# Optimization experiments

Hardware: AMD Instinct MI355X
Metric: run time of the kernel (lower is better)

Reference implementation:

```python
import jax, jax.numpy as jnp
import numpy as np

N_NODES = 50000
NEG_SLOPE = 0.2


def gat_conv(x, src, dst, W, a_src, a_dst, bias, heads):
    # x: [N, Fin]; W: [Fin, heads*C]; a_src/a_dst: [heads, C]; bias: [heads*C]
    n = x.shape[0]
    h = (x @ W).reshape(n, heads, -1)              # [N, H, C]
    alpha_src = jnp.einsum('nhc,hc->nh', h, a_src)  # [N, H]
    alpha_dst = jnp.einsum('nhc,hc->nh', h, a_dst)  # [N, H]
    e = alpha_src[src] + alpha_dst[dst]             # [E, H]
    e = jax.nn.leaky_relu(e, NEG_SLOPE)
    # segment softmax over edges grouped by destination node
    m = jax.ops.segment_max(e, dst, num_segments=n)          # [N, H]
    e = jnp.exp(e - jax.lax.stop_gradient(m)[dst])
    s = jax.ops.segment_sum(e, dst, num_segments=n)          # [N, H]
    alpha = e / (s[dst] + 1e-16)                              # [E, H]
    msg = h[src] * alpha[:, :, None]                          # [E, H, C]
    out = jax.ops.segment_sum(msg, dst, num_segments=n)      # [N, H, C]
    return out.reshape(n, -1) + bias


def add_self_loops(edge_index, n):
    loops = jnp.arange(n, dtype=edge_index.dtype)
    src = jnp.concatenate([edge_index[0], loops])
    dst = jnp.concatenate([edge_index[1], loops])
    return src, dst


def setup_inputs() -> dict:
    key = jax.random.key(0)
    ks = jax.random.split(key, 10)
    num_features, num_classes, heads1, c1 = 128, 40, 8, 32
    n_edges = 800000
    x = jax.random.normal(ks[0], (N_NODES, num_features), dtype=jnp.float32)
    edge_index = jax.random.randint(ks[1], (2, n_edges), 0, N_NODES, dtype=jnp.int64)
    sc = 0.1
    W1 = jax.random.normal(ks[2], (num_features, heads1 * c1), dtype=jnp.float32) * sc
    a_src1 = jax.random.normal(ks[3], (heads1, c1), dtype=jnp.float32) * sc
    a_dst1 = jax.random.normal(ks[4], (heads1, c1), dtype=jnp.float32) * sc
    b1 = jnp.zeros((heads1 * c1,), dtype=jnp.float32)
    W2 = jax.random.normal(ks[5], (heads1 * c1, num_classes), dtype=jnp.float32) * sc
    a_src2 = jax.random.normal(ks[6], (1, num_classes), dtype=jnp.float32) * sc
    a_dst2 = jax.random.normal(ks[7], (1, num_classes), dtype=jnp.float32) * sc
    b2 = jnp.zeros((num_classes,), dtype=jnp.float32)
    return {"x": x, "edge_index": edge_index, "W1": W1, "a_src1": a_src1,
            "a_dst1": a_dst1, "b1": b1, "W2": W2, "a_src2": a_src2,
            "a_dst2": a_dst2, "b2": b2}


def reference(x, edge_index, W1, a_src1, a_dst1, b1, W2, a_src2, a_dst2, b2):
    src, dst = add_self_loops(edge_index, x.shape[0])
    h = gat_conv(x, src, dst, W1, a_src1, a_dst1, b1, heads=8)
    h = jax.nn.elu(h)
    h = gat_conv(h, src, dst, W2, a_src2, a_dst2, b2, heads=1)
    return jax.nn.log_softmax(h, axis=1)
```

## Files before the change

kernel.cpp:

```cpp
#include <hip/hip_runtime.h>
#include <math.h>

#define NNODES 50000
#define F_IN   128
#define F1     256
#define H1N    8
#define NCLS   40
#define NEG    0.2f
#define MNEG  -3.0e38f
#define SCAN_BLOCKS 196

typedef unsigned int uint32;
typedef __attribute__((ext_vector_type(8))) short short8v;
typedef __attribute__((ext_vector_type(4))) float f32x4;

__device__ __forceinline__ float leaky(float x) { return x > 0.f ? x : NEG * x; }

__device__ __forceinline__ unsigned short f2bf(float f) {
  uint32 u = __float_as_uint(f);
  u = (u + 0x7FFFu + ((u >> 16) & 1u)) >> 16;
  return (unsigned short)u;
}
__device__ __forceinline__ float bf_lo(uint32 u) { return __uint_as_float(u << 16); }
__device__ __forceinline__ float bf_hi(uint32 u) { return __uint_as_float(u & 0xFFFF0000u); }

__global__ __launch_bounds__(256) void convx_k(const float* __restrict__ x,
                                               unsigned short* __restrict__ xb) {
  int i = blockIdx.x * 256 + threadIdx.x;
  float4 v = ((const float4*)x)[i];
  uint2 o;
  o.x = (uint32)f2bf(v.x) | ((uint32)f2bf(v.y) << 16);
  o.y = (uint32)f2bf(v.z) | ((uint32)f2bf(v.w) << 16);
  ((uint2*)xb)[i] = o;
}

__global__ __launch_bounds__(256) void convw_k(const float* __restrict__ W,
                                               unsigned short* __restrict__ Wt) {
  int id = blockIdx.x * 256 + threadIdx.x;
  int k = id >> 8, c = id & 255;
  Wt[c * 128 + k] = f2bf(W[id]);
}

__global__ __launch_bounds__(256) void convw2_k(const float* __restrict__ W2,
                                                unsigned short* __restrict__ Wt2) {
  int id = blockIdx.x * 256 + threadIdx.x;
  int c = id >> 8, k = id & 255;
  Wt2[c * 256 + k] = (c < NCLS) ? f2bf(W2[k * NCLS + c]) : (unsigned short)0;
}

__global__ __launch_bounds__(256) void gemm1_mfma_k(
    const unsigned short* __restrict__ xb, const unsigned short* __restrict__ Wt,
    const float* __restrict__ asrc, const float* __restrict__ adst,
    unsigned short* __restrict__ h1b, float* __restrict__ as1,
    float* __restrict__ ad1) {
  const int lane = threadIdx.x & 63;
  const int wv   = threadIdx.x >> 6;
  const int row0 = blockIdx.x * 64 + wv * 16;
  if (row0 >= NNODES) return;
  const int lrow = lane & 15;
  const int kgrp = lane >> 4;

  const short8v* xp = (const short8v*)xb;
  short8v a[4];
  #pragma unroll
  for (int ks = 0; ks < 4; ++ks)
    a[ks] = xp[(row0 + lrow) * 16 + ks * 4 + kgrp];

  const short8v* wp = (const short8v*)Wt;
  float ps[4] = {0.f, 0.f, 0.f, 0.f};
  float pd[4] = {0.f, 0.f, 0.f, 0.f};

  for (int n = 0; n < 16; ++n) {
    f32x4 acc = {0.f, 0.f, 0.f, 0.f};
    #pragma unroll
    for (int ks = 0; ks < 4; ++ks) {
      short8v b = wp[(n * 16 + lrow) * 16 + ks * 4 + kgrp];
      acc = __builtin_amdgcn_mfma_f32_16x16x32_bf16(a[ks], b, acc, 0, 0, 0);
    }
    const int col = n * 16 + lrow;
    const float ascv = asrc[col];
    const float advv = adst[col];
    #pragma unroll
    for (int r = 0; r < 4; ++r) {
      int row = row0 + kgrp * 4 + r;
      h1b[(long)row * F1 + col] = f2bf(acc[r]);
      ps[r] = fmaf(acc[r], ascv, ps[r]);
      pd[r] = fmaf(acc[r], advv, pd[r]);
    }
    if (n & 1) {
      const int head = n >> 1;
      #pragma unroll
      for (int r = 0; r < 4; ++r) {
        #pragma unroll
        for (int mask = 1; mask <= 8; mask <<= 1) {
          ps[r] += __shfl_xor(ps[r], mask, 64);
          pd[r] += __shfl_xor(pd[r], mask, 64);
        }
      }
      if (lrow == 0) {
        #pragma unroll
        for (int r = 0; r < 4; ++r) {
          int row = row0 + kgrp * 4 + r;
          as1[row * H1N + head] = ps[r];
          ad1[row * H1N + head] = pd[r];
        }
      }
      #pragma unroll
      for (int r = 0; r < 4; ++r) { ps[r] = 0.f; pd[r] = 0.f; }
    }
  }
}

__global__ __launch_bounds__(256) void hist_k(const int* __restrict__ ei,
                                              int* __restrict__ deg, int E, int ET) {
  int e = blockIdx.x * 256 + threadIdx.x;
  if (e >= ET) return;
  int d = (e < E) ? ei[E + e] : e - E;
  atomicAdd(&deg[d], 1);
}

__global__ __launch_bounds__(256) void partsum_k(const int* __restrict__ deg,
                                                 int* __restrict__ blocksum) {
  int idx = blockIdx.x * 256 + threadIdx.x;
  int v = (idx < NNODES) ? deg[idx] : 0;
  #pragma unroll
  for (int m = 32; m >= 1; m >>= 1) v += __shfl_xor(v, m, 64);
  __shared__ int sh[4];
  if ((threadIdx.x & 63) == 0) sh[threadIdx.x >> 6] = v;
  __syncthreads();
  if (threadIdx.x == 0) blocksum[blockIdx.x] = sh[0] + sh[1] + sh[2] + sh[3];
}

__global__ __launch_bounds__(256) void scanblocks_k(const int* __restrict__ blocksum,
                                                    int* __restrict__ blockoff) {
  __shared__ int sh[256];
  int t = threadIdx.x;
  int v = (t < SCAN_BLOCKS) ? blocksum[t] : 0;
  sh[t] = v;
  __syncthreads();
  for (int off = 1; off < 256; off <<= 1) {
    int u = (t >= off) ? sh[t - off] : 0;
    __syncthreads();
    sh[t] += u;
    __syncthreads();
  }
  if (t < SCAN_BLOCKS) blockoff[t] = (t == 0) ? 0 : sh[t - 1];
}

__global__ __launch_bounds__(256) void rowstart_k(const int* __restrict__ deg,
                                                  const int* __restrict__ blockoff,
                                                  int* __restrict__ row_start,
                                                  int* __restrict__ cursor, int ET) {
  __shared__ int sh[256];
  int t = threadIdx.x;
  int idx = blockIdx.x * 256 + t;
  int v = (idx < NNODES) ? deg[idx] : 0;
  sh[t] = v;
  __syncthreads();
  for (int off = 1; off < 256; off <<= 1) {
    int u = (t >= off) ? sh[t - off] : 0;
    __syncthreads();
    sh[t] += u;
    __syncthreads();
  }
  int incl = sh[t];
  int base = blockoff[blockIdx.x];
  if (idx < NNODES) {
    int rs = base + incl - v;
    row_start[idx] = rs;
    cursor[idx] = rs;
    if (idx == NNODES - 1) row_start[NNODES] = base + incl;
  }
}

__global__ __launch_bounds__(256) void scatter_k(const int* __restrict__ ei,
                                                 int* __restrict__ cursor,
                                                 int* __restrict__ csr_src, int E, int ET) {
  int e = blockIdx.x * 256 + threadIdx.x;
  if (e >= ET) return;
  int s, d;
  if (e < E) { s = ei[e]; d = ei[E + e]; } else { s = d = e - E; }
  int pos = atomicAdd(&cursor[d], 1);
  csr_src[pos] = s;
}

__global__ __launch_bounds__(256) void att1_k(
    const int* __restrict__ row_start, const int* __restrict__ csr_src,
    const float* __restrict__ as1, const float* __restrict__ ad1,
    float* __restrict__ alpha1, float* __restrict__ r1) {
  int wave = threadIdx.x >> 6, lane = threadIdx.x & 63;
  int d = blockIdx.x * 4 + wave;
  if (d >= NNODES) return;
  int r0 = row_start[d], r1e = row_start[d + 1];
  float adv[8];
  #pragma unroll
  for (int h = 0; h < 8; ++h) adv[h] = ad1[d * 8 + h];
  float sum[8];
  #pragma unroll
  for (int h = 0; h < 8; ++h) sum[h] = 0.f;
  for (int i = r0 + lane; i < r1e; i += 64) {
    int s = csr_src[i];
    const float4* ap = (const float4*)(as1 + (long)s * 8);
    float4 a0 = ap[0], a1 = ap[1];
    float av[8] = {a0.x, a0.y, a0.z, a0.w, a1.x, a1.y, a1.z, a1.w};
    float ex[8];
    #pragma unroll
    for (int h = 0; h < 8; ++h) {
      ex[h] = __expf(leaky(av[h] + adv[h]));
      sum[h] += ex[h];
    }
    float4* op = (float4*)(alpha1 + (long)i * 8);
    op[0] = make_float4(ex[0], ex[1], ex[2], ex[3]);
    op[1] = make_float4(ex[4], ex[5], ex[6], ex[7]);
  }
  #pragma unroll
  for (int mask = 1; mask <= 32; mask <<= 1) {
    #pragma unroll
    for (int h = 0; h < 8; ++h) sum[h] += __shfl_xor(sum[h], mask, 64);
  }
  if (lane == 0) {
    #pragma unroll
    for (int h = 0; h < 8; ++h) r1[d * 8 + h] = 1.f / (sum[h] + 1e-16f);
  }
}

__global__ __launch_bounds__(128) void agg1_k(
    const int* __restrict__ row_start, const int* __restrict__ csr_src,
    const float* __restrict__ alpha1, const float* __restrict__ r1,
    const uint32* __restrict__ h1b, const float* __restrict__ b1,
    uint32* __restrict__ x2b) {
  int d = blockIdx.x;
  int t = threadIdx.x;
  int h = t >> 4;
  int r0 = row_start[d], r1e = row_start[d + 1];
  float acc0 = 0.f, acc1 = 0.f;
  int i = r0;
  for (; i + 2 <= r1e; i += 2) {
    int s0 = csr_src[i], s1 = csr_src[i + 1];
    float a0 = alpha1[(long)i * 8 + h];
    float a1 = alpha1[(long)(i + 1) * 8 + h];
    uint32 v0 = h1b[s0 * 128 + t];
    uint32 v1 = h1b[s1 * 128 + t];
    acc0 = fmaf(bf_lo(v0), a0, acc0);
    acc1 = fmaf(bf_hi(v0), a0, acc1);
    acc0 = fmaf(bf_lo(v1), a1, acc0);
    acc1 = fmaf(bf_hi(v1), a1, acc1);
  }
  if (i < r1e) {
    int s0 = csr_src[i];
    float a0 = alpha1[(long)i * 8 + h];
    uint32 v0 = h1b[s0 * 128 + t];
    acc0 = fmaf(bf_lo(v0), a0, acc0);
    acc1 = fmaf(bf_hi(v0), a0, acc1);
  }
  float rch = r1[d * 8 + h];
  acc0 *= rch;
  acc1 *= rch;
  float2 b = ((const float2*)b1)[t];
  float o0 = acc0 + b.x, o1 = acc1 + b.y;
  o0 = o0 > 0.f ? o0 : expm1f(o0);
  o1 = o1 > 0.f ? o1 : expm1f(o1);
  x2b[(long)d * 128 + t] = (uint32)f2bf(o0) | ((uint32)f2bf(o1) << 16);
}

__global__ __launch_bounds__(256) void gemm2_mfma_k(
    const unsigned short* __restrict__ x2b, const unsigned short* __restrict__ Wt2,
    const float* __restrict__ a_src2, const float* __restrict__ a_dst2,
    float* __restrict__ h2, float* __restrict__ as2, float* __restrict__ ad2) {
  const int lane = threadIdx.x & 63;
  const int wv   = threadIdx.x >> 6;
  const int row0 = blockIdx.x * 64 + wv * 16;
  if (row0 >= NNODES) return;
  const int lrow = lane & 15;
  const int kgrp = lane >> 4;

  const short8v* xp = (const short8v*)x2b;
  short8v a[8];
  #pragma unroll
  for (int ks = 0; ks < 8; ++ks)
    a[ks] = xp[(row0 + lrow) * 32 + ks * 4 + kgrp];

  const short8v* wp = (const short8v*)Wt2;
  float ps[4] = {0.f, 0.f, 0.f, 0.f};
  float pd[4] = {0.f, 0.f, 0.f, 0.f};

  #pragma unroll
  for (int n = 0; n < 3; ++n) {
    f32x4 acc = {0.f, 0.f, 0.f, 0.f};
    #pragma unroll
    for (int ks = 0; ks < 8; ++ks) {
      short8v b = wp[(n * 16 + lrow) * 32 + ks * 4 + kgrp];
      acc = __builtin_amdgcn_mfma_f32_16x16x32_bf16(a[ks], b, acc, 0, 0, 0);
    }
    const int col = n * 16 + lrow;
    const bool valid = col < NCLS;
    const float asv = valid ? a_src2[col] : 0.f;
    const float adv = valid ? a_dst2[col] : 0.f;
    #pragma unroll
    for (int r = 0; r < 4; ++r) {
      int row = row0 + kgrp * 4 + r;
      if (valid) h2[(long)row * NCLS + col] = acc[r];
      ps[r] = fmaf(acc[r], asv, ps[r]);
      pd[r] = fmaf(acc[r], adv, pd[r]);
    }
  }
  #pragma unroll
  for (int r = 0; r < 4; ++r) {
    #pragma unroll
    for (int mask = 1; mask <= 8; mask <<= 1) {
      ps[r] += __shfl_xor(ps[r], mask, 64);
      pd[r] += __shfl_xor(pd[r], mask, 64);
    }
  }
  if (lrow == 0) {
    #pragma unroll
    for (int r = 0; r < 4; ++r) {
      int row = row0 + kgrp * 4 + r;
      as2[row] = ps[r];
      ad2[row] = pd[r];
    }
  }
}

__global__ __launch_bounds__(256) void att2e_k(
    const int* __restrict__ row_start, const int* __restrict__ csr_src,
    const float* __restrict__ as2, const float* __restrict__ ad2,
    float* __restrict__ alpha2, float* __restrict__ r2) {
  int wave = threadIdx.x >> 6, lane = threadIdx.x & 63;
  int d = blockIdx.x * 4 + wave;
  if (d >= NNODES) return;
  int r0 = row_start[d], r1e = row_start[d + 1];
  float add = ad2[d];
  float sum = 0.f;
  for (int i = r0 + lane; i < r1e; i += 64) {
    float ex = __expf(leaky(as2[csr_src[i]] + add));
    alpha2[i] = ex;
    sum += ex;
  }
  #pragma unroll
  for (int mask = 1; mask <= 32; mask <<= 1) sum += __shfl_xor(sum, mask, 64);
  if (lane == 0) r2[d] = 1.f / (sum + 1e-16f);
}

__global__ __launch_bounds__(256) void agg2_k(
    const int* __restrict__ row_start, const int* __restrict__ csr_src,
    const float* __restrict__ alpha2, const float* __restrict__ r2,
    const float* __restrict__ h2, const float* __restrict__ b2,
    float* __restrict__ out) {
  int wave = threadIdx.x >> 6, lane = threadIdx.x & 63;
  int d = blockIdx.x * 4 + wave;
  if (d >= NNODES) return;
  int r0 = row_start[d], r1e = row_start[d + 1];

  float acc = 0.f;
  int i = r0;
  for (; i + 2 <= r1e; i += 2) {
    int s0 = csr_src[i], s1 = csr_src[i + 1];
    float a0 = alpha2[i], a1 = alpha2[i + 1];
    float v0 = (lane < NCLS) ? h2[(long)s0 * NCLS + lane] : 0.f;
    float v1 = (lane < NCLS) ? h2[(long)s1 * NCLS + lane] : 0.f;
    acc = fmaf(v0, a0, acc);
    acc = fmaf(v1, a1, acc);
  }
  if (i < r1e) {
    int s0 = csr_src[i];
    float a0 = alpha2[i];
    float v0 = (lane < NCLS) ? h2[(long)s0 * NCLS + lane] : 0.f;
    acc = fmaf(v0, a0, acc);
  }
  acc *= r2[d];

  float v = (lane < NCLS) ? acc + b2[lane] : MNEG;
  float mm = v;
  #pragma unroll
  for (int mask = 1; mask <= 32; mask <<= 1) mm = fmaxf(mm, __shfl_xor(mm, mask, 64));
  float ex = (lane < NCLS) ? __expf(v - mm) : 0.f;
  float se = ex;
  #pragma unroll
  for (int mask = 1; mask <= 32; mask <<= 1) se += __shfl_xor(se, mask, 64);
  if (lane < NCLS) out[(long)d * NCLS + lane] = v - mm - __logf(se);
}

extern "C" void kernel_launch(void* const* d_in, const int* in_sizes, int n_in,
                              void* d_out, int out_size, void* d_ws, size_t ws_size,
                              hipStream_t stream) {
  const float* x      = (const float*)d_in[0];
  const int*   ei     = (const int*)d_in[1];
  const float* W1     = (const float*)d_in[2];
  const float* a_src1 = (const float*)d_in[3];
  const float* a_dst1 = (const float*)d_in[4];
  const float* b1     = (const float*)d_in[5];
  const float* W2     = (const float*)d_in[6];
  const float* a_src2 = (const float*)d_in[7];
  const float* a_dst2 = (const float*)d_in[8];
  const float* b2     = (const float*)d_in[9];
  float* out = (float*)d_out;

  const int E  = in_sizes[1] / 2;
  const int ET = E + NNODES;

  float* ws = (float*)d_ws;
  unsigned short* h1b = (unsigned short*)ws;
  float* h2     = ws;
  float* as2    = ws + 2000000;
  float* ad2    = ws + 2050000;
  uint32* x2b   = (uint32*)(ws + 6400000);
  unsigned short* xb = (unsigned short*)(ws + 9700000);
  unsigned short* Wt = (unsigned short*)(ws + 13000000);
  unsigned short* Wt2 = (unsigned short*)(ws + 13100000);
  float* alpha2 = ws + 13200000;
  float* r1     = ws + 15000000;
  float* r2     = ws + 15400000;
  float* as1    = ws + 19200000;
  float* ad1    = ws + 19600000;
  float* alpha1 = ws + 20000000;
  int* row_start = (int*)(ws + 26800000);
  int* cursor    = row_start + 50001;
  int* deg       = cursor + 50000;
  int* csr_src   = deg + 50000;
  int* blocksum  = csr_src + 850000;
  int* blockoff  = blocksum + 256;

  hipMemsetAsync(deg, 0, NNODES * sizeof(int), stream);

  hist_k<<<(ET + 255) / 256, 256, 0, stream>>>(ei, deg, E, ET);
  partsum_k<<<SCAN_BLOCKS, 256, 0, stream>>>(deg, blocksum);
  scanblocks_k<<<1, 256, 0, stream>>>(blocksum, blockoff);
  rowstart_k<<<SCAN_BLOCKS, 256, 0, stream>>>(deg, blockoff, row_start, cursor, ET);
  scatter_k<<<(ET + 255) / 256, 256, 0, stream>>>(ei, cursor, csr_src, E, ET);

  convx_k<<<6250, 256, 0, stream>>>(x, xb);
  convw_k<<<128, 256, 0, stream>>>(W1, Wt);
  convw2_k<<<48, 256, 0, stream>>>(W2, Wt2);
  gemm1_mfma_k<<<(NNODES + 63) / 64, 256, 0, stream>>>(xb, Wt, a_src1, a_dst1,
                                                       h1b, as1, ad1);
  att1_k<<<NNODES / 4, 256, 0, stream>>>(row_start, csr_src, as1, ad1, alpha1, r1);
  agg1_k<<<NNODES, 128, 0, stream>>>(row_start, csr_src, alpha1, r1,
                                     (const uint32*)h1b, b1, x2b);

  gemm2_mfma_k<<<(NNODES + 63) / 64, 256, 0, stream>>>(
      (const unsigned short*)x2b, Wt2, a_src2, a_dst2, h2, as2, ad2);
  att2e_k<<<NNODES / 4, 256, 0, stream>>>(row_start, csr_src, as2, ad2, alpha2, r2);
  agg2_k<<<NNODES / 4, 256, 0, stream>>>(row_start, csr_src, alpha2, r2, h2, b2, out);
}
```

Measured before the change: 424.7 us.

## Fuse attention softmax into aggregation kernels, recomputing edge weights on the fly

The separate attention kernels for both GAT layers are removed. Each aggregation kernel now computes the per-destination softmax denominator itself, using a block reduction through LDS for layer 1 and a wave shuffle for layer 2. It then recomputes exp(leaky(as[s]+ad[d])) per edge during accumulation instead of reading stored alpha arrays. This drops the alpha1/alpha2 writes and reads (about 850K×8 floats for layer 1) and two kernel launches. In exchange it adds redundant exp computation, an extra pass over edges with gathers of as1/as2, and two __syncthreads per node in agg1.

```diff
diff --git a/kernel.cpp b/kernel.cpp
--- a/kernel.cpp
+++ b/kernel.cpp
@@ -184,61 +184,42 @@
   csr_src[pos] = s;
 }
 
-__global__ __launch_bounds__(256) void att1_k(
+__global__ __launch_bounds__(128) void agg1_k(
     const int* __restrict__ row_start, const int* __restrict__ csr_src,
     const float* __restrict__ as1, const float* __restrict__ ad1,
-    float* __restrict__ alpha1, float* __restrict__ r1) {
-  int wave = threadIdx.x >> 6, lane = threadIdx.x & 63;
-  int d = blockIdx.x * 4 + wave;
-  if (d >= NNODES) return;
-  int r0 = row_start[d], r1e = row_start[d + 1];
-  float adv[8];
-  #pragma unroll
-  for (int h = 0; h < 8; ++h) adv[h] = ad1[d * 8 + h];
-  float sum[8];
-  #pragma unroll
-  for (int h = 0; h < 8; ++h) sum[h] = 0.f;
-  for (int i = r0 + lane; i < r1e; i += 64) {
-    int s = csr_src[i];
-    const float4* ap = (const float4*)(as1 + (long)s * 8);
-    float4 a0 = ap[0], a1 = ap[1];
-    float av[8] = {a0.x, a0.y, a0.z, a0.w, a1.x, a1.y, a1.z, a1.w};
-    float ex[8];
-    #pragma unroll
-    for (int h = 0; h < 8; ++h) {
-      ex[h] = __expf(leaky(av[h] + adv[h]));
-      sum[h] += ex[h];
-    }
-    float4* op = (float4*)(alpha1 + (long)i * 8);
-    op[0] = make_float4(ex[0], ex[1], ex[2], ex[3]);
-    op[1] = make_float4(ex[4], ex[5], ex[6], ex[7]);
-  }
-  #pragma unroll
-  for (int mask = 1; mask <= 32; mask <<= 1) {
-    #pragma unroll
-    for (int h = 0; h < 8; ++h) sum[h] += __shfl_xor(sum[h], mask, 64);
-  }
-  if (lane == 0) {
-    #pragma unroll
-    for (int h = 0; h < 8; ++h) r1[d * 8 + h] = 1.f / (sum[h] + 1e-16f);
-  }
-}
-
-__global__ __launch_bounds__(128) void agg1_k(
-    const int* __restrict__ row_start, const int* __restrict__ csr_src,
-    const float* __restrict__ alpha1, const float* __restrict__ r1,
     const uint32* __restrict__ h1b, const float* __restrict__ b1,
     uint32* __restrict__ x2b) {
-  int d = blockIdx.x;
-  int t = threadIdx.x;
-  int h = t >> 4;
-  int r0 = row_start[d], r1e = row_start[d + 1];
+  __shared__ float partial[128];
+  __shared__ float rs_lds[8];
+  const int d = blockIdx.x;
+  const int t = threadIdx.x;
+  const int r0 = row_start[d], r1e = row_start[d + 1];
+
+  {
+    const int hh = t & 7, slot = t >> 3;
+    const float adv = ad1[d * 8 + hh];
+    float sum = 0.f;
+    for (int i = r0 + slot; i < r1e; i += 16)
+      sum += __expf(leaky(as1[csr_src[i] * 8 + hh] + adv));
+    partial[t] = sum;
+  }
+  __syncthreads();
+  if (t < 8) {
+    float s = 0.f;
+    #pragma unroll
+    for (int j = 0; j < 16; ++j) s += partial[t + 8 * j];
+    rs_lds[t] = 1.f / (s + 1e-16f);
+  }
+  __syncthreads();
+
+  const int h = t >> 4;
+  const float adh = ad1[d * 8 + h];
   float acc0 = 0.f, acc1 = 0.f;
   int i = r0;
   for (; i + 2 <= r1e; i += 2) {
     int s0 = csr_src[i], s1 = csr_src[i + 1];
-    float a0 = alpha1[(long)i * 8 + h];
-    float a1 = alpha1[(long)(i + 1) * 8 + h];
+    float a0 = __expf(leaky(as1[s0 * 8 + h] + adh));
+    float a1 = __expf(leaky(as1[s1 * 8 + h] + adh));
     uint32 v0 = h1b[s0 * 128 + t];
     uint32 v1 = h1b[s1 * 128 + t];
     acc0 = fmaf(bf_lo(v0), a0, acc0);
@@ -248,12 +229,12 @@
   }
   if (i < r1e) {
     int s0 = csr_src[i];
-    float a0 = alpha1[(long)i * 8 + h];
+    float a0 = __expf(leaky(as1[s0 * 8 + h] + adh));
     uint32 v0 = h1b[s0 * 128 + t];
     acc0 = fmaf(bf_lo(v0), a0, acc0);
     acc1 = fmaf(bf_hi(v0), a0, acc1);
   }
-  float rch = r1[d * 8 + h];
+  float rch = rs_lds[h];
   acc0 *= rch;
   acc1 *= rch;
   float2 b = ((const float2*)b1)[t];
@@ -322,41 +303,30 @@
   }
 }
 
-__global__ __launch_bounds__(256) void att2e_k(
+__global__ __launch_bounds__(256) void agg2_k(
     const int* __restrict__ row_start, const int* __restrict__ csr_src,
     const float* __restrict__ as2, const float* __restrict__ ad2,
-    float* __restrict__ alpha2, float* __restrict__ r2) {
-  int wave = threadIdx.x >> 6, lane = threadIdx.x & 63;
-  int d = blockIdx.x * 4 + wave;
-  if (d >= NNODES) return;
-  int r0 = row_start[d], r1e = row_start[d + 1];
-  float add = ad2[d];
-  float sum = 0.f;
-  for (int i = r0 + lane; i < r1e; i += 64) {
-    float ex = __expf(leaky(as2[csr_src[i]] + add));
-    alpha2[i] = ex;
-    sum += ex;
-  }
-  #pragma unroll
-  for (int mask = 1; mask <= 32; mask <<= 1) sum += __shfl_xor(sum, mask, 64);
-  if (lane == 0) r2[d] = 1.f / (sum + 1e-16f);
-}
-
-__global__ __launch_bounds__(256) void agg2_k(
-    const int* __restrict__ row_start, const int* __restrict__ csr_src,
-    const float* __restrict__ alpha2, const float* __restrict__ r2,
     const float* __restrict__ h2, const float* __restrict__ b2,
     float* __restrict__ out) {
   int wave = threadIdx.x >> 6, lane = threadIdx.x & 63;
   int d = blockIdx.x * 4 + wave;
   if (d >= NNODES) return;
   int r0 = row_start[d], r1e = row_start[d + 1];
+  const float add = ad2[d];
+
+  float sum = 0.f;
+  for (int i = r0 + lane; i < r1e; i += 64)
+    sum += __expf(leaky(as2[csr_src[i]] + add));
+  #pragma unroll
+  for (int mask = 1; mask <= 32; mask <<= 1) sum += __shfl_xor(sum, mask, 64);
+  float rcp = 1.f / (sum + 1e-16f);
 
   float acc = 0.f;
   int i = r0;
   for (; i + 2 <= r1e; i += 2) {
     int s0 = csr_src[i], s1 = csr_src[i + 1];
-    float a0 = alpha2[i], a1 = alpha2[i + 1];
+    float a0 = __expf(leaky(as2[s0] + add));
+    float a1 = __expf(leaky(as2[s1] + add));
     float v0 = (lane < NCLS) ? h2[(long)s0 * NCLS + lane] : 0.f;
     float v1 = (lane < NCLS) ? h2[(long)s1 * NCLS + lane] : 0.f;
     acc = fmaf(v0, a0, acc);
@@ -364,11 +334,11 @@
   }
   if (i < r1e) {
     int s0 = csr_src[i];
-    float a0 = alpha2[i];
+    float a0 = __expf(leaky(as2[s0] + add));
     float v0 = (lane < NCLS) ? h2[(long)s0 * NCLS + lane] : 0.f;
     acc = fmaf(v0, a0, acc);
   }
-  acc *= r2[d];
+  acc *= rcp;
 
   float v = (lane < NCLS) ? acc + b2[lane] : MNEG;
   float mm = v;
@@ -408,12 +378,8 @@
   unsigned short* xb = (unsigned short*)(ws + 9700000);
   unsigned short* Wt = (unsigned short*)(ws + 13000000);
   unsigned short* Wt2 = (unsigned short*)(ws + 13100000);
-  float* alpha2 = ws + 13200000;
-  float* r1     = ws + 15000000;
-  float* r2     = ws + 15400000;
   float* as1    = ws + 19200000;
   float* ad1    = ws + 19600000;
-  float* alpha1 = ws + 20000000;
   int* row_start = (int*)(ws + 26800000);
   int* cursor    = row_start + 50001;
   int* deg       = cursor + 50000;
@@ -434,12 +400,10 @@
   convw2_k<<<48, 256, 0, stream>>>(W2, Wt2);
   gemm1_mfma_k<<<(NNODES + 63) / 64, 256, 0, stream>>>(xb, Wt, a_src1, a_dst1,
                                                        h1b, as1, ad1);
-  att1_k<<<NNODES / 4, 256, 0, stream>>>(row_start, csr_src, as1, ad1, alpha1, r1);
-  agg1_k<<<NNODES, 128, 0, stream>>>(row_start, csr_src, alpha1, r1,
+  agg1_k<<<NNODES, 128, 0, stream>>>(row_start, csr_src, as1, ad1,
                                      (const uint32*)h1b, b1, x2b);
 
   gemm2_mfma_k<<<(NNODES + 63) / 64, 256, 0, stream>>>(
       (const unsigned short*)x2b, Wt2, a_src2, a_dst2, h2, as2, ad2);
-  att2e_k<<<NNODES / 4, 256, 0, stream>>>(row_start, csr_src, as2, ad2, alpha2, r2);
-  agg2_k<<<NNODES / 4, 256, 0, stream>>>(row_start, csr_src, alpha2, r2, h2, b2, out);
-}
+  agg2_k<<<NNODES / 4, 256, 0, stream>>>(row_start, csr_src, as2, ad2, h2, b2, out);
+}
```

New measurement: 409.4 us. -3.6%, faster.
